# Performance work log

Hardware: AMD Instinct MI355X
Metric: run time of the kernel (lower is better)

Reference implementation:

```python
import jax, jax.numpy as jnp
import numpy as np

B, T, C = 8192, 240, 16
DAYS, STRIDE = 10, 10
EPS_BN = 1e-5   # nn.BatchNorm1d default eps
EPS = 1e-8      # guard for corr/zscore denominators


def setup_inputs() -> dict:
    key = jax.random.key(0)
    k1, k2, k3 = jax.random.split(key, 3)
    # prices/features are positive in this repo; shift uniform to [0.5, 1.5]
    x = jax.random.uniform(k1, (B, T, C), jnp.float32) + 0.5
    pair = C * (C - 1) // 2
    out_ch = pair * 2 + C * 5  # 320
    gamma = jax.random.uniform(k2, (out_ch,), jnp.float32, 0.5, 1.5)
    beta = jax.random.normal(k3, (out_ch,), jnp.float32) * 0.1
    return {"x": x, "gamma": gamma, "beta": beta}


def _features(x):
    """Seven rolling-window extractors, concatenated on the feature axis.
    x: (B, T, C) -> (B, W, 2*P + 5*C) with W = (T-DAYS)//STRIDE + 1."""
    Bx, Tx, Cx = x.shape
    starts = jnp.arange(0, Tx - DAYS + 1, STRIDE)
    win = x[:, starts[:, None] + jnp.arange(DAYS), :]        # (B, W, D, C)
    mean = win.mean(axis=2)                                   # TS_Mean (B, W, C)
    dx = win - mean[:, :, None, :]
    var = (dx * dx).mean(axis=2)                              # population var
    std = jnp.sqrt(var)                                       # TS_Stddev
    ii, jj = jnp.triu_indices(Cx, k=1)                        # channel pairs i<j
    cov = (dx[..., ii] * dx[..., jj]).mean(axis=2)            # TS_Cov (B, W, P)
    corr = cov / (std[..., ii] * std[..., jj] + EPS)          # TS_Corr
    zscore = mean / (std + EPS)                               # TS_Zscore
    ret = win[:, :, -1, :] / win[:, :, 0, :] - 1.0            # TS_Return
    w = jnp.arange(1, DAYS + 1, dtype=x.dtype) / (DAYS * (DAYS + 1) / 2)
    decay = jnp.einsum('bwdc,d->bwc', win, w)                 # TS_Decaylinear
    return jnp.concatenate([corr, cov, std, zscore, ret, decay, mean], axis=2)


def reference(x, gamma, beta):
    f = _features(x)                                          # (B, W, 320)
    # per-branch BatchNorm1d (training-mode batch stats) == per-channel BN on concat
    m = f.mean(axis=(0, 1))
    v = ((f - m) ** 2).mean(axis=(0, 1))
    return (f - m) / jnp.sqrt(v + EPS_BN) * gamma + beta
```

## Files before the change

kernel.cpp:

```cpp
#include <hip/hip_runtime.h>

#define NROWS   196608
#define NTILES_TOTAL 12288
#define OUTC    320
#define R_      16
#define WSTRIDE 164
#define CV_S    20
#define FB_S    20
#define EPS_F   1e-8f
#define EPS_BN  1e-5f
#define RA_BLOCKS 768

__device__ __forceinline__ int pair_idx(int i, int j) {
    return i * 15 - (i * (i - 1)) / 2 + j - i - 1;
}

__device__ const unsigned char PIJ[120] = {
    0x01,0x02,0x03,0x04,0x05,0x06,0x07,0x08,0x09,0x0A,0x0B,0x0C,0x0D,0x0E,0x0F,
    0x12,0x13,0x14,0x15,0x16,0x17,0x18,0x19,0x1A,0x1B,0x1C,0x1D,0x1E,0x1F,
    0x23,0x24,0x25,0x26,0x27,0x28,0x29,0x2A,0x2B,0x2C,0x2D,0x2E,0x2F,
    0x34,0x35,0x36,0x37,0x38,0x39,0x3A,0x3B,0x3C,0x3D,0x3E,0x3F,
    0x45,0x46,0x47,0x48,0x49,0x4A,0x4B,0x4C,0x4D,0x4E,0x4F,
    0x56,0x57,0x58,0x59,0x5A,0x5B,0x5C,0x5D,0x5E,0x5F,
    0x67,0x68,0x69,0x6A,0x6B,0x6C,0x6D,0x6E,0x6F,
    0x78,0x79,0x7A,0x7B,0x7C,0x7D,0x7E,0x7F,
    0x89,0x8A,0x8B,0x8C,0x8D,0x8E,0x8F,
    0x9A,0x9B,0x9C,0x9D,0x9E,0x9F,
    0xAB,0xAC,0xAD,0xAE,0xAF,
    0xBC,0xBD,0xBE,0xBF,
    0xCD,0xCE,0xCF,
    0xDE,0xDF,
    0xEF
};

template<int MODE, int NTILES>
__global__ __launch_bounds__(320)
void fe_kernel(const float* __restrict__ x, float* __restrict__ dst,
               const float* __restrict__ ab) {
    __shared__ __align__(16) float win[R_ * WSTRIDE];
    __shared__ __align__(16) float cv2[120 * CV_S];
    __shared__ __align__(16) float featB[80 * FB_S];

    const int t = threadIdx.x;

    const int c = t;
    int pi = 0, pj = 0, pp = 0;
    if (c < 240) {
        pp = (c < 120) ? c : (c - 120);
        int b = PIJ[pp];
        pi = b >> 4; pj = b & 15;
    }
    const int c2 = c - 240;

    float scale = 0.f, shift = 0.f;
    if (MODE == 1) { scale = ab[c]; shift = ab[c + OUTC]; }

    float acc = 0.f, acc2 = 0.f;
    float accB = 0.f, accB2 = 0.f;

#pragma unroll 1
    for (int tt = 0; tt < NTILES; ++tt) {
        const int tile = blockIdx.x * NTILES + tt;
        const float4* src = reinterpret_cast<const float4*>(x) + (size_t)tile * 640;

        __syncthreads();
#pragma unroll
        for (int k = 0; k < 2; ++k) {
            int q = t + k * 320;
            float4 v = src[q];
            int row = q / 40, pos = q % 40;
            reinterpret_cast<float4*>(win)[row * (WSTRIDE / 4) + pos] = v;
        }
        __syncthreads();

        if (t < 160) {
            const int r = t & 15, q = t >> 4;
            const float* wr = win + r * WSTRIDE;
            if (q < 6) {
                const int i0 = (q < 3) ? 0 : ((q < 5) ? 4 : 8);
                const int j0 = (q == 0) ? 4 : ((q == 1 || q == 3) ? 8 : 12);
                float gacc[4][4];
#pragma unroll
                for (int a = 0; a < 4; ++a)
#pragma unroll
                    for (int b = 0; b < 4; ++b) gacc[a][b] = 0.f;
#pragma unroll
                for (int d = 0; d < 10; ++d) {
                    float4 vi = *reinterpret_cast<const float4*>(wr + d * 16 + i0);
                    float4 vj = *reinterpret_cast<const float4*>(wr + d * 16 + j0);
                    float ai[4] = {vi.x, vi.y, vi.z, vi.w};
                    float aj[4] = {vj.x, vj.y, vj.z, vj.w};
#pragma unroll
                    for (int a = 0; a < 4; ++a)
#pragma unroll
                        for (int b = 0; b < 4; ++b)
                            gacc[a][b] += ai[a] * aj[b];
                }
#pragma unroll
                for (int a = 0; a < 4; ++a) {
                    int i = i0 + a;
                    int base = i * 15 - (i * (i - 1)) / 2 - i - 1;
#pragma unroll
                    for (int b = 0; b < 4; ++b)
                        cv2[(base + j0 + b) * CV_S + r] = gacc[a][b] * 0.1f;
                }
            } else {
                const int i0 = (q - 6) << 2;
                float g01 = 0.f, g02 = 0.f, g03 = 0.f,
                      g12 = 0.f, g13 = 0.f, g23 = 0.f;
#pragma unroll
                for (int d = 0; d < 10; ++d) {
                    float4 vi = *reinterpret_cast<const float4*>(wr + d * 16 + i0);
                    float a0 = vi.x, a1 = vi.y, a2 = vi.z, a3 = vi.w;
                    g01 += a0 * a1; g02 += a0 * a2; g03 += a0 * a3;
                    g12 += a1 * a2; g13 += a1 * a3; g23 += a2 * a3;
                }
                cv2[pair_idx(i0 + 0, i0 + 1) * CV_S + r] = g01 * 0.1f;
                cv2[pair_idx(i0 + 0, i0 + 2) * CV_S + r] = g02 * 0.1f;
                cv2[pair_idx(i0 + 0, i0 + 3) * CV_S + r] = g03 * 0.1f;
                cv2[pair_idx(i0 + 1, i0 + 2) * CV_S + r] = g12 * 0.1f;
                cv2[pair_idx(i0 + 1, i0 + 3) * CV_S + r] = g13 * 0.1f;
                cv2[pair_idx(i0 + 2, i0 + 3) * CV_S + r] = g23 * 0.1f;
            }
        } else if (t >= 256) {
            const int lane = t - 256;
            const int r = lane & 15;
            const int c0 = (lane >> 4) << 2;
            const float* wr = win + r * WSTRIDE + c0;
            float sm[4], sq[4], dec[4], first[4], last[4];
#pragma unroll
            for (int k = 0; k < 4; ++k) { sm[k] = 0.f; sq[k] = 0.f; dec[k] = 0.f; }
#pragma unroll
            for (int d = 0; d < 10; ++d) {
                float4 v = *reinterpret_cast<const float4*>(wr + d * 16);
                float a[4] = {v.x, v.y, v.z, v.w};
#pragma unroll
                for (int k = 0; k < 4; ++k) {
                    sm[k] += a[k];
                    sq[k] += a[k] * a[k];
                    dec[k] += a[k] * (float)(d + 1);
                    if (d == 0) first[k] = a[k];
                    if (d == 9) last[k]  = a[k];
                }
            }
#pragma unroll
            for (int k = 0; k < 4; ++k) {
                int ch = c0 + k;
                float m = sm[k] * 0.1f;
                float var = fmaxf(sq[k] * 0.1f - m * m, 0.f);
                float s = sqrtf(var);
                featB[(0 * 16 + ch) * FB_S + r] = s;
                featB[(1 * 16 + ch) * FB_S + r] = m / (s + EPS_F);
                featB[(2 * 16 + ch) * FB_S + r] = last[k] / first[k] - 1.f;
                featB[(3 * 16 + ch) * FB_S + r] = dec[k] * (1.f / 55.f);
                featB[(4 * 16 + ch) * FB_S + r] = m;
            }
        }
        __syncthreads();

        if (MODE == 0 && c >= 120 && c < 240) {
        } else {
#pragma unroll
            for (int rb4 = 0; rb4 < 4; ++rb4) {
                const int rb = rb4 * 4;
                if (c < 120) {
                    float4 g4  = *reinterpret_cast<const float4*>(cv2 + pp * CV_S + rb);
                    float4 mi4 = *reinterpret_cast<const float4*>(featB + (64 + pi) * FB_S + rb);
                    float4 mj4 = *reinterpret_cast<const float4*>(featB + (64 + pj) * FB_S + rb);
                    float4 si4 = *reinterpret_cast<const float4*>(featB + pi * FB_S + rb);
                    float4 sj4 = *reinterpret_cast<const float4*>(featB + pj * FB_S + rb);
                    float g[4]  = {g4.x, g4.y, g4.z, g4.w};
                    float mi[4] = {mi4.x, mi4.y, mi4.z, mi4.w};
                    float mj[4] = {mj4.x, mj4.y, mj4.z, mj4.w};
                    float si[4] = {si4.x, si4.y, si4.z, si4.w};
                    float sj[4] = {sj4.x, sj4.y, sj4.z, sj4.w};
#pragma unroll
                    for (int k = 0; k < 4; ++k) {
                        float num = g[k] - mi[k] * mj[k];
                        float cr  = num / (si[k] * sj[k] + EPS_F);
                        if (MODE == 1) {
                            dst[(size_t)tile * (R_ * OUTC) + (rb + k) * OUTC + c]
                                = cr * scale + shift;
                        } else {
                            acc += cr;  acc2 += cr * cr;
                            accB += num; accB2 += num * num;
                        }
                    }
                } else if (c < 240) {
                    float4 g4  = *reinterpret_cast<const float4*>(cv2 + pp * CV_S + rb);
                    float4 mi4 = *reinterpret_cast<const float4*>(featB + (64 + pi) * FB_S + rb);
                    float4 mj4 = *reinterpret_cast<const float4*>(featB + (64 + pj) * FB_S + rb);
                    float g[4]  = {g4.x, g4.y, g4.z, g4.w};
                    float mi[4] = {mi4.x, mi4.y, mi4.z, mi4.w};
                    float mj[4] = {mj4.x, mj4.y, mj4.z, mj4.w};
#pragma unroll
                    for (int k = 0; k < 4; ++k) {
                        float num = g[k] - mi[k] * mj[k];
                        dst[(size_t)tile * (R_ * OUTC) + (rb + k) * OUTC + c]
                            = num * scale + shift;
                    }
                } else {
                    float4 f4 = *reinterpret_cast<const float4*>(featB + c2 * FB_S + rb);
                    float vals[4] = {f4.x, f4.y, f4.z, f4.w};
#pragma unroll
                    for (int k = 0; k < 4; ++k) {
                        if (MODE == 1) {
                            dst[(size_t)tile * (R_ * OUTC) + (rb + k) * OUTC + c]
                                = vals[k] * scale + shift;
                        } else {
                            acc += vals[k]; acc2 += vals[k] * vals[k];
                        }
                    }
                }
            }
        }
    }

    if (MODE == 0) {
        float* db = dst + (size_t)blockIdx.x * 640;
        if (c < 120) {
            db[c]         = acc;   db[c + 320] = acc2;
            db[c + 120]   = accB;  db[c + 440] = accB2;
        } else if (c >= 240) {
            db[c]         = acc;   db[c + 320] = acc2;
        }
    }
}

__global__ __launch_bounds__(256)
void reduceA_kernel(const float* __restrict__ part1, float* __restrict__ part2,
                    int nb) {
    const int rows = nb / RA_BLOCKS;
    const int b = blockIdx.x;
    for (int v = threadIdx.x; v < 640; v += 256) {
        float s = 0.f;
        for (int j = 0; j < rows; ++j)
            s += part1[(size_t)(b + RA_BLOCKS * j) * 640 + v];
        part2[(size_t)b * 640 + v] = s;
    }
}

__global__ __launch_bounds__(256)
void finalize_kernel(const float* __restrict__ part2,
                     const float* __restrict__ gamma,
                     const float* __restrict__ beta,
                     float* __restrict__ ab) {
    __shared__ double rs[256], rs2[256];
    const int c = blockIdx.x, t = threadIdx.x;
    double s = 0.0, s2 = 0.0;
    for (int r = t; r < RA_BLOCKS; r += 256) {
        s  += (double)part2[(size_t)r * 640 + c];
        s2 += (double)part2[(size_t)r * 640 + c + OUTC];
    }
    rs[t] = s; rs2[t] = s2;
    __syncthreads();
    for (int off = 128; off; off >>= 1) {
        if (t < off) { rs[t] += rs[t + off]; rs2[t] += rs2[t + off]; }
        __syncthreads();
    }
    if (t == 0) {
        const double invN = 1.0 / (double)NROWS;
        double m = rs[0] * invN;
        double v = rs2[0] * invN - m * m;
        if (v < 0.0) v = 0.0;
        float a = gamma[c] / sqrtf((float)v + EPS_BN);
        ab[c] = a;
        ab[OUTC + c] = beta[c] - (float)m * a;
    }
}

extern "C" void kernel_launch(void* const* d_in, const int* in_sizes, int n_in,
                              void* d_out, int out_size, void* d_ws, size_t ws_size,
                              hipStream_t stream) {
    const float* x     = (const float*)d_in[0];
    const float* gamma = (const float*)d_in[1];
    const float* beta  = (const float*)d_in[2];
    float* out = (float*)d_out;

    const size_t need1 = (size_t)NTILES_TOTAL * 640 * 4
                       + (size_t)RA_BLOCKS * 640 * 4 + 640 * 4;
    const int nb = (need1 <= ws_size) ? NTILES_TOTAL : (NTILES_TOTAL / 8);

    float* part1 = (float*)d_ws;
    float* part2 = part1 + (size_t)nb * 640;
    float* ab    = part2 + (size_t)RA_BLOCKS * 640;

    if (nb == NTILES_TOTAL)
        fe_kernel<0, 1><<<nb, 320, 0, stream>>>(x, part1, nullptr);
    else
        fe_kernel<0, 8><<<nb, 320, 0, stream>>>(x, part1, nullptr);
    reduceA_kernel<<<RA_BLOCKS, 256, 0, stream>>>(part1, part2, nb);
    finalize_kernel<<<OUTC, 256, 0, stream>>>(part2, gamma, beta, ab);
    fe_kernel<1, 1><<<NTILES_TOTAL, 320, 0, stream>>>(x, out, ab);
}
```

Measured before the change: 131.8 us.

## Fuse stats, finalize and apply passes into one cooperative persistent kernel

Replaces the four-launch pipeline (stats pass, partial reduce, finalize, apply pass) with a single cooperative persistent kernel that uses grid-wide syncs between phases. Each block loops over several tiles and prefetches the next tile's input into registers while computing the current one. The per-channel BN finalize now runs inside the kernel, with double reductions done by one block per channel. This removes the launch gaps and the large partial-sum workspace traffic, at the cost of two grid syncs and a grid size limited by occupancy.

```diff
diff --git a/kernel.cpp b/kernel.cpp
--- a/kernel.cpp
+++ b/kernel.cpp
@@ -1,4 +1,7 @@
 #include <hip/hip_runtime.h>
+#include <hip/hip_cooperative_groups.h>
+
+namespace cg = cooperative_groups;
 
 #define NROWS   196608
 #define NTILES_TOTAL 12288
@@ -33,6 +36,249 @@
     0xEF
 };
 
+__global__ __launch_bounds__(320, 4)
+void fused_kernel(const float* __restrict__ x,
+                  const float* __restrict__ gamma,
+                  const float* __restrict__ beta,
+                  float* __restrict__ out,
+                  float* __restrict__ part1,
+                  float* __restrict__ abuf,
+                  int ntiles, int nblocks) {
+    __shared__ __align__(16) float win[R_ * WSTRIDE];
+    __shared__ __align__(16) float cv2[120 * CV_S];
+    __shared__ __align__(16) float featB[80 * FB_S];
+    __shared__ double rsd[256], rsd2[256];
+
+    const int t = threadIdx.x;
+    const int c = t;
+    int pi = 0, pj = 0, pp = 0;
+    if (c < 240) {
+        pp = (c < 120) ? c : (c - 120);
+        int b = PIJ[pp];
+        pi = b >> 4; pj = b & 15;
+    }
+    const int c2 = c - 240;
+    const int base = blockIdx.x * ntiles;
+
+    float acc = 0.f, acc2 = 0.f;
+    float accB = 0.f, accB2 = 0.f;
+    float scale = 0.f, shift = 0.f;
+
+    float4 pf0, pf1;
+    auto load_pf = [&](int tile) {
+        const float4* s = reinterpret_cast<const float4*>(x) + (size_t)tile * 640;
+        pf0 = s[t]; pf1 = s[t + 320];
+    };
+
+    auto run_pass = [&](bool apply) {
+        if (base < NTILES_TOTAL) load_pf(base);
+#pragma unroll 1
+        for (int tt = 0; tt < ntiles; ++tt) {
+            const int tile = base + tt;
+            const bool valid = tile < NTILES_TOTAL;
+            __syncthreads();
+            if (valid) {
+                const int q0 = t, q1 = t + 320;
+                reinterpret_cast<float4*>(win)[(q0 / 40) * (WSTRIDE / 4) + (q0 % 40)] = pf0;
+                reinterpret_cast<float4*>(win)[(q1 / 40) * (WSTRIDE / 4) + (q1 % 40)] = pf1;
+            }
+            if (tt + 1 < ntiles && tile + 1 < NTILES_TOTAL) load_pf(tile + 1);
+            __syncthreads();
+
+            if (valid) {
+                if (t < 160) {
+                    const int r = t & 15, q = t >> 4;
+                    const float* wr = win + r * WSTRIDE;
+                    if (q < 6) {
+                        const int i0 = (q < 3) ? 0 : ((q < 5) ? 4 : 8);
+                        const int j0 = (q == 0) ? 4 : ((q == 1 || q == 3) ? 8 : 12);
+                        float gacc[4][4];
+#pragma unroll
+                        for (int a = 0; a < 4; ++a)
+#pragma unroll
+                            for (int b = 0; b < 4; ++b) gacc[a][b] = 0.f;
+#pragma unroll
+                        for (int d = 0; d < 10; ++d) {
+                            float4 vi = *reinterpret_cast<const float4*>(wr + d * 16 + i0);
+                            float4 vj = *reinterpret_cast<const float4*>(wr + d * 16 + j0);
+                            float ai[4] = {vi.x, vi.y, vi.z, vi.w};
+                            float aj[4] = {vj.x, vj.y, vj.z, vj.w};
+#pragma unroll
+                            for (int a = 0; a < 4; ++a)
+#pragma unroll
+                                for (int b = 0; b < 4; ++b)
+                                    gacc[a][b] += ai[a] * aj[b];
+                        }
+#pragma unroll
+                        for (int a = 0; a < 4; ++a) {
+                            int i = i0 + a;
+                            int bs = i * 15 - (i * (i - 1)) / 2 - i - 1;
+#pragma unroll
+                            for (int b = 0; b < 4; ++b)
+                                cv2[(bs + j0 + b) * CV_S + r] = gacc[a][b] * 0.1f;
+                        }
+                    } else {
+                        const int i0 = (q - 6) << 2;
+                        float g01 = 0.f, g02 = 0.f, g03 = 0.f,
+                              g12 = 0.f, g13 = 0.f, g23 = 0.f;
+#pragma unroll
+                        for (int d = 0; d < 10; ++d) {
+                            float4 vi = *reinterpret_cast<const float4*>(wr + d * 16 + i0);
+                            float a0 = vi.x, a1 = vi.y, a2 = vi.z, a3 = vi.w;
+                            g01 += a0 * a1; g02 += a0 * a2; g03 += a0 * a3;
+                            g12 += a1 * a2; g13 += a1 * a3; g23 += a2 * a3;
+                        }
+                        cv2[pair_idx(i0 + 0, i0 + 1) * CV_S + r] = g01 * 0.1f;
+                        cv2[pair_idx(i0 + 0, i0 + 2) * CV_S + r] = g02 * 0.1f;
+                        cv2[pair_idx(i0 + 0, i0 + 3) * CV_S + r] = g03 * 0.1f;
+                        cv2[pair_idx(i0 + 1, i0 + 2) * CV_S + r] = g12 * 0.1f;
+                        cv2[pair_idx(i0 + 1, i0 + 3) * CV_S + r] = g13 * 0.1f;
+                        cv2[pair_idx(i0 + 2, i0 + 3) * CV_S + r] = g23 * 0.1f;
+                    }
+                } else if (t >= 256) {
+                    const int lane = t - 256;
+                    const int r = lane & 15;
+                    const int c0 = (lane >> 4) << 2;
+                    const float* wr = win + r * WSTRIDE + c0;
+                    float sm[4], sq[4], dec[4], first[4], last[4];
+#pragma unroll
+                    for (int k = 0; k < 4; ++k) { sm[k] = 0.f; sq[k] = 0.f; dec[k] = 0.f; }
+#pragma unroll
+                    for (int d = 0; d < 10; ++d) {
+                        float4 v = *reinterpret_cast<const float4*>(wr + d * 16);
+                        float a[4] = {v.x, v.y, v.z, v.w};
+#pragma unroll
+                        for (int k = 0; k < 4; ++k) {
+                            sm[k] += a[k];
+                            sq[k] += a[k] * a[k];
+                            dec[k] += a[k] * (float)(d + 1);
+                            if (d == 0) first[k] = a[k];
+                            if (d == 9) last[k]  = a[k];
+                        }
+                    }
+#pragma unroll
+                    for (int k = 0; k < 4; ++k) {
+                        int ch = c0 + k;
+                        float m = sm[k] * 0.1f;
+                        float var = fmaxf(sq[k] * 0.1f - m * m, 0.f);
+                        float s = sqrtf(var);
+                        featB[(0 * 16 + ch) * FB_S + r] = s;
+                        featB[(1 * 16 + ch) * FB_S + r] = m / (s + EPS_F);
+                        featB[(2 * 16 + ch) * FB_S + r] = last[k] / first[k] - 1.f;
+                        featB[(3 * 16 + ch) * FB_S + r] = dec[k] * (1.f / 55.f);
+                        featB[(4 * 16 + ch) * FB_S + r] = m;
+                    }
+                }
+            }
+            __syncthreads();
+
+            if (valid) {
+                if (!apply && c >= 120 && c < 240) {
+                } else {
+#pragma unroll
+                    for (int rb4 = 0; rb4 < 4; ++rb4) {
+                        const int rb = rb4 * 4;
+                        if (c < 120) {
+                            float4 g4  = *reinterpret_cast<const float4*>(cv2 + pp * CV_S + rb);
+                            float4 mi4 = *reinterpret_cast<const float4*>(featB + (64 + pi) * FB_S + rb);
+                            float4 mj4 = *reinterpret_cast<const float4*>(featB + (64 + pj) * FB_S + rb);
+                            float4 si4 = *reinterpret_cast<const float4*>(featB + pi * FB_S + rb);
+                            float4 sj4 = *reinterpret_cast<const float4*>(featB + pj * FB_S + rb);
+                            float g[4]  = {g4.x, g4.y, g4.z, g4.w};
+                            float mi[4] = {mi4.x, mi4.y, mi4.z, mi4.w};
+                            float mj[4] = {mj4.x, mj4.y, mj4.z, mj4.w};
+                            float si[4] = {si4.x, si4.y, si4.z, si4.w};
+                            float sj[4] = {sj4.x, sj4.y, sj4.z, sj4.w};
+#pragma unroll
+                            for (int k = 0; k < 4; ++k) {
+                                float num = g[k] - mi[k] * mj[k];
+                                float cr  = num / (si[k] * sj[k] + EPS_F);
+                                if (apply) {
+                                    out[(size_t)tile * (R_ * OUTC) + (rb + k) * OUTC + c]
+                                        = cr * scale + shift;
+                                } else {
+                                    acc += cr;  acc2 += cr * cr;
+                                    accB += num; accB2 += num * num;
+                                }
+                            }
+                        } else if (c < 240) {
+                            float4 g4  = *reinterpret_cast<const float4*>(cv2 + pp * CV_S + rb);
+                            float4 mi4 = *reinterpret_cast<const float4*>(featB + (64 + pi) * FB_S + rb);
+                            float4 mj4 = *reinterpret_cast<const float4*>(featB + (64 + pj) * FB_S + rb);
+                            float g[4]  = {g4.x, g4.y, g4.z, g4.w};
+                            float mi[4] = {mi4.x, mi4.y, mi4.z, mi4.w};
+                            float mj[4] = {mj4.x, mj4.y, mj4.z, mj4.w};
+#pragma unroll
+                            for (int k = 0; k < 4; ++k) {
+                                float num = g[k] - mi[k] * mj[k];
+                                out[(size_t)tile * (R_ * OUTC) + (rb + k) * OUTC + c]
+                                    = num * scale + shift;
+                            }
+                        } else {
+                            float4 f4 = *reinterpret_cast<const float4*>(featB + c2 * FB_S + rb);
+                            float vals[4] = {f4.x, f4.y, f4.z, f4.w};
+#pragma unroll
+                            for (int k = 0; k < 4; ++k) {
+                                if (apply) {
+                                    out[(size_t)tile * (R_ * OUTC) + (rb + k) * OUTC + c]
+                                        = vals[k] * scale + shift;
+                                } else {
+                                    acc += vals[k]; acc2 += vals[k] * vals[k];
+                                }
+                            }
+                        }
+                    }
+                }
+            }
+        }
+    };
+
+    run_pass(false);
+    {
+        float* db = part1 + (size_t)blockIdx.x * 640;
+        if (c < 120) {
+            db[c]       = acc;   db[c + 320] = acc2;
+            db[c + 120] = accB;  db[c + 440] = accB2;
+        } else if (c >= 240) {
+            db[c]       = acc;   db[c + 320] = acc2;
+        }
+    }
+    __threadfence();
+    cg::this_grid().sync();
+
+    if (blockIdx.x < OUTC) {
+        const int ch = blockIdx.x;
+        if (t < 256) {
+            double s = 0.0, s2 = 0.0;
+            for (int r = t; r < nblocks; r += 256) {
+                s  += (double)part1[(size_t)r * 640 + ch];
+                s2 += (double)part1[(size_t)r * 640 + ch + OUTC];
+            }
+            rsd[t] = s; rsd2[t] = s2;
+        }
+        __syncthreads();
+        for (int off = 128; off; off >>= 1) {
+            if (t < off) { rsd[t] += rsd[t + off]; rsd2[t] += rsd2[t + off]; }
+            __syncthreads();
+        }
+        if (t == 0) {
+            const double invN = 1.0 / (double)NROWS;
+            double m = rsd[0] * invN;
+            double v = rsd2[0] * invN - m * m;
+            if (v < 0.0) v = 0.0;
+            float a = gamma[ch] / sqrtf((float)v + EPS_BN);
+            abuf[ch] = a;
+            abuf[ch + OUTC] = beta[ch] - (float)m * a;
+        }
+    }
+    __threadfence();
+    cg::this_grid().sync();
+
+    scale = abuf[c];
+    shift = abuf[c + OUTC];
+    run_pass(true);
+}
+
 template<int MODE, int NTILES>
 __global__ __launch_bounds__(320)
 void fe_kernel(const float* __restrict__ x, float* __restrict__ dst,
@@ -42,7 +288,6 @@
     __shared__ __align__(16) float featB[80 * FB_S];
 
     const int t = threadIdx.x;
-
     const int c = t;
     int pi = 0, pj = 0, pp = 0;
     if (c < 240) {
@@ -99,10 +344,10 @@
 #pragma unroll
                 for (int a = 0; a < 4; ++a) {
                     int i = i0 + a;
-                    int base = i * 15 - (i * (i - 1)) / 2 - i - 1;
+                    int bs = i * 15 - (i * (i - 1)) / 2 - i - 1;
 #pragma unroll
                     for (int b = 0; b < 4; ++b)
-                        cv2[(base + j0 + b) * CV_S + r] = gacc[a][b] * 0.1f;
+                        cv2[(bs + j0 + b) * CV_S + r] = gacc[a][b] * 0.1f;
                 }
             } else {
                 const int i0 = (q - 6) << 2;
@@ -219,10 +464,10 @@
     if (MODE == 0) {
         float* db = dst + (size_t)blockIdx.x * 640;
         if (c < 120) {
-            db[c]         = acc;   db[c + 320] = acc2;
-            db[c + 120]   = accB;  db[c + 440] = accB2;
+            db[c]       = acc;   db[c + 320] = acc2;
+            db[c + 120] = accB;  db[c + 440] = accB2;
         } else if (c >= 240) {
-            db[c]         = acc;   db[c + 320] = acc2;
+            db[c]       = acc;   db[c + 320] = acc2;
         }
     }
 }
@@ -277,6 +522,33 @@
     const float* beta  = (const float*)d_in[2];
     float* out = (float*)d_out;
 
+    int dev = 0;
+    (void)hipGetDevice(&dev);
+    int coop = 0;
+    (void)hipDeviceGetAttribute(&coop, hipDeviceAttributeCooperativeLaunch, dev);
+    int nsm = 0;
+    (void)hipDeviceGetAttribute(&nsm, hipDeviceAttributeMultiprocessorCount, dev);
+    int blocks_per_cu = 0;
+    (void)hipOccupancyMaxActiveBlocksPerMultiprocessor(
+        &blocks_per_cu, (const void*)fused_kernel, 320, 0);
+
+    long grid_l = (long)blocks_per_cu * (long)nsm;
+    if (grid_l > NTILES_TOTAL) grid_l = NTILES_TOTAL;
+    const int grid = (int)grid_l;
+    const size_t coop_ws_need = ((size_t)grid * 640 + 640) * sizeof(float);
+
+    if (coop && grid >= OUTC && coop_ws_need <= ws_size) {
+        int ntiles = (NTILES_TOTAL + grid - 1) / grid;
+        float* part1 = (float*)d_ws;
+        float* abuf  = part1 + (size_t)grid * 640;
+        int nblocks = grid;
+        void* args[] = {(void*)&x, (void*)&gamma, (void*)&beta, (void*)&out,
+                        (void*)&part1, (void*)&abuf, (void*)&ntiles, (void*)&nblocks};
+        hipError_t err = hipLaunchCooperativeKernel(
+            (const void*)fused_kernel, dim3(grid), dim3(320), args, 0, stream);
+        if (err == hipSuccess) return;
+    }
+
     const size_t need1 = (size_t)NTILES_TOTAL * 640 * 4
                        + (size_t)RA_BLOCKS * 640 * 4 + 640 * 4;
     const int nb = (need1 <= ws_size) ? NTILES_TOTAL : (NTILES_TOTAL / 8);
```

After: 381.3 us. 189% more time.
